# Performance work log

Hardware: AMD Instinct MI355X
Metric: run time of the kernel (lower is better)

The kernel has to match this reference:

```python
import jax, jax.numpy as jnp
from jax import lax
import numpy as np

B, L, D = 2048, 100, 64      # batch, max_len, embedding_dim
K = 64                       # embedding_num (codebook entries)
CB = K * 8                   # code_book_dim = 512 (== D*8 encoder out channels)
ITEMS = 1_000_000
EPS = 1e-3                   # tf.layers.batch_normalization default epsilon


def setup_inputs() -> dict:
    key = jax.random.key(0)
    ks = jax.random.split(key, 16)
    w = lambda i, shape: jax.random.normal(ks[i], shape, dtype=jnp.float32) * 0.05
    z = lambda c: jnp.zeros((c,), jnp.float32)
    o = lambda c: jnp.ones((c,), jnp.float32)
    return {
        "history_item_ids": jax.random.randint(ks[0], (B, L), 0, ITEMS, dtype=jnp.int32),
        "history_item_masks": jax.random.randint(ks[1], (B, L), 0, 2, dtype=jnp.int32),
        "item_embedding_table": jax.random.normal(ks[2], (ITEMS, D), dtype=jnp.float32),
        "user_book": jax.random.normal(ks[3], (K, CB), dtype=jnp.float32),
        "e_w1": w(4, (2, 2, D, 2 * D)), "e_b1": z(2 * D), "e_g1": o(2 * D), "e_be1": z(2 * D),
        "e_w2": w(5, (2, 2, 2 * D, 4 * D)), "e_b2": z(4 * D), "e_g2": o(4 * D), "e_be2": z(4 * D),
        "e_w3": w(6, (2, 2, 4 * D, 8 * D)), "e_b3": z(8 * D),
        "d_w1": w(7, (2, 2, 8 * D, 4 * D)), "d_b1": z(4 * D), "d_g1": o(4 * D), "d_be1": z(4 * D),
        "d_w2": w(8, (2, 2, 4 * D, 2 * D)), "d_b2": z(2 * D), "d_g2": o(2 * D), "d_be2": z(2 * D),
        "d_w3": w(9, (2, 2, 2 * D, D)), "d_b3": z(D),
    }


def _forward(history_item_ids, history_item_masks, item_embedding_table, user_book,
             e_w1, e_b1, e_g1, e_be1, e_w2, e_b2, e_g2, e_be2, e_w3, e_b3,
             d_w1, d_b1, d_g1, d_be1, d_w2, d_b2, d_g2, d_be2, d_w3, d_b3):
    dn = ('NHWC', 'HWIO', 'NHWC')
    bn = lambda x, g, b: x * (g / jnp.sqrt(1.0 + EPS)) + b  # inference BN: moving mean 0, var 1
    conv = lambda x, w_, b_: lax.conv_general_dilated(x, w_, (1, 1), 'VALID', dimension_numbers=dn) + b_
    deconv = lambda x, w_, b_: lax.conv_transpose(x, w_, (1, 1), 'VALID', dimension_numbers=dn) + b_

    mask = (history_item_masks >= 1).astype(jnp.float32)               # [B,L]
    hist = item_embedding_table[history_item_ids] * mask[..., None]    # [B,L,D]

    H = int(L ** 0.5); W = L // H
    h = hist.reshape(-1, H, W, D)
    h = jax.nn.relu(bn(conv(h, e_w1, e_b1), e_g1, e_be1))              # [B,9,9,2D]
    h = jax.nn.relu(bn(conv(h, e_w2, e_b2), e_g2, e_be2))              # [B,8,8,4D]
    x_encode = conv(h, e_w3, e_b3)                                     # [B,7,7,CB]

    # nearest-neighbor codebook lookup (get_quantized)
    flat = x_encode.reshape(-1, CB)                                    # [B*49,CB]
    dist = ((flat * flat).sum(1, keepdims=True)
            + (user_book * user_book).sum(1)
            - 2.0 * flat @ user_book.T)                                # [B*49,K]
    idx = jnp.argmin(dist, axis=1)
    quantized = user_book[idx].reshape(x_encode.shape)                 # [B,7,7,CB]

    # straight-through estimator
    st = x_encode + lax.stop_gradient(quantized - x_encode)
    g = jax.nn.relu(bn(deconv(st, d_w1, d_b1), d_g1, d_be1))           # [B,8,8,4D]
    g = jax.nn.relu(bn(deconv(g, d_w2, d_b2), d_g2, d_be2))            # [B,9,9,2D]
    vq_x = deconv(g, d_w3, d_b3).reshape(hist.shape)                   # [B,L,D]

    vq_mean = vq_x.sum(1) / mask.sum(-1, keepdims=True)                # [B,D]
    mse = lambda a, b: jnp.mean((a - b) ** 2)
    beta = 0.25
    vqvae_loss = (mse(hist, vq_x)
                  + mse(quantized, lax.stop_gradient(x_encode))
                  + beta * mse(x_encode, lax.stop_gradient(quantized)))
    return vq_mean, vq_x, vqvae_loss


def reference(history_item_ids, history_item_masks, item_embedding_table, user_book,
              e_w1, e_b1, e_g1, e_be1, e_w2, e_b2, e_g2, e_be2, e_w3, e_b3,
              d_w1, d_b1, d_g1, d_be1, d_w2, d_b2, d_g2, d_be2, d_w3, d_b3):
    return _forward(history_item_ids, history_item_masks, item_embedding_table, user_book,
                    e_w1, e_b1, e_g1, e_be1, e_w2, e_b2, e_g2, e_be2, e_w3, e_b3,
                    d_w1, d_b1, d_g1, d_be1, d_w2, d_b2, d_g2, d_be2, d_w3, d_b3)
```

## Files before the change

### kernel.cpp

```cpp
#include <hip/hip_runtime.h>
#include <hip/hip_bf16.h>
#include <cstdint>
#include <cstddef>


typedef __attribute__((ext_vector_type(8))) short short8v;
typedef __attribute__((ext_vector_type(4))) float f32x4;

constexpr int B  = 2048;
constexpr int L  = 100;
constexpr int K  = 64;
constexpr int CB = 512;
#define MARGIN 0.1f

constexpr size_t R0_OFF  = 0;
constexpr size_t R1_OFF  = 51380224;
constexpr size_t IDX_OFF = 84934656;
constexpr size_t CBN_OFF = 85035008;
constexpr size_t CNT_OFF = 85035072;
constexpr size_t ACC_OFF = 85035088;
constexpr size_t WL_OFF  = 85035104;
constexpr size_t WB_OFF  = 85135456;

constexpr size_t EW1H=0,       EW1L=32768;
constexpr size_t EW2H=65536,   EW2L=196608;
constexpr size_t EW3H=327680;
constexpr size_t DW2H=851968,  DW3H=983040;
constexpr size_t W3BH=1015808, W3BL=1081344;
constexpr size_t WB_USH_END=1146880;

constexpr size_t BW1_OFF  = WB_OFF + 573440;
constexpr size_t DOTB_OFF = BW1_OFF + 65536;

__device__ inline ushort bf16_hi(float f){ __hip_bfloat16 h=__float2bfloat16(f); return *(ushort*)&h; }
__device__ inline float  bf16_tof(ushort u){ __hip_bfloat16 h; *(ushort*)&h=u; return __bfloat162float(h); }

__device__ void wtrans(const float* __restrict__ w, int IC, int OC,
                       ushort* __restrict__ hi, ushort* __restrict__ lo,
                       int gid, int gsz)
{
    int tot = 4*IC*OC;
    for (int i = gid; i < tot; i += gsz) {
        int kk = i/(IC*OC), r = i - kk*(IC*OC), ic = r/OC, oc = r - ic*OC;
        float v = w[i];
        ushort h = bf16_hi(v);
        size_t dst = ((size_t)kk*OC + oc)*IC + ic;
        hi[dst] = h;
        if (lo) lo[dst] = bf16_hi(v - bf16_tof(h));
    }
}

__global__ __launch_bounds__(256)
void wprep_k(const float* e1, const float* e2, const float* e3,
             const float* d2, const float* d3, ushort* wb)
{
    int gid = blockIdx.x*256 + threadIdx.x, gsz = gridDim.x*256;
    wtrans(e1,  64, 128, wb+EW1H, wb+EW1L, gid, gsz);
    wtrans(e2, 128, 256, wb+EW2H, wb+EW2L, gid, gsz);
    wtrans(e3, 256, 512, wb+EW3H, nullptr, gid, gsz);
    wtrans(d2, 256, 128, wb+DW2H, nullptr, gid, gsz);
    wtrans(d3, 128,  64, wb+DW3H, nullptr, gid, gsz);
}

__global__ __launch_bounds__(256)
void w3b_k(const float* __restrict__ e_w3, const float* __restrict__ book,
           ushort* __restrict__ wb)
{
    const int kk = blockIdx.x >> 6, k = blockIdx.x & 63, ic = threadIdx.x;
    const float4* wr = (const float4*)(e_w3 + ((size_t)(kk*256)+ic)*512);
    const float4* br = (const float4*)(book + (size_t)k*512);
    float s = 0.f;
    for (int c = 0; c < 128; ++c) {
        float4 a = wr[c], bb = br[c];
        s = fmaf(a.x,bb.x,fmaf(a.y,bb.y,fmaf(a.z,bb.z,fmaf(a.w,bb.w,s))));
    }
    size_t dst = ((size_t)(kk*64+k))*256 + ic;
    ushort h = bf16_hi(s);
    wb[W3BH+dst] = h;
    wb[W3BL+dst] = bf16_hi(s - bf16_tof(h));
}

__global__ __launch_bounds__(256)
void bw1_k(const float* __restrict__ d_w1, const float* __restrict__ book,
           float* __restrict__ bw1)
{
    const int tap = blockIdx.x >> 6, k = blockIdx.x & 63, oc = threadIdx.x;
    const float* br = book + (size_t)k*512;
    const float* wr = d_w1 + (size_t)(tap*512)*256 + oc;
    float s = 0.f;
    for (int ic = 0; ic < 512; ++ic)
        s = fmaf(br[ic], wr[(size_t)ic*256], s);
    bw1[((size_t)(tap*64+k))*256 + oc] = s;
}

__global__ __launch_bounds__(256)
void prep_k(const float* __restrict__ book, const float* __restrict__ e_b3,
            float* __restrict__ cbn, float* __restrict__ dotb,
            float* __restrict__ acc, int* __restrict__ cnt)
{
    const int t = threadIdx.x;
    if (t < 64) {
        const float* r = book + t * 512;
        float s = 0.f, d = 0.f;
        for (int c = 0; c < 512; ++c) { s = fmaf(r[c], r[c], s); d = fmaf(e_b3[c], r[c], d); }
        cbn[t] = s; dotb[t] = d;
    }
    if (t == 64 || t == 65) acc[t-64] = 0.f;
    if (t == 66) *cnt = 0;
}

template<int IH,int IW,int IC,int OC,int PAD,int MODE,bool HASBN,bool SPLIT,
         int OCS,int ICC,int MT,int OUTFMT,bool FUSE>
__global__ __launch_bounds__(256)
void sconv_k(const uint* __restrict__ in_pk, const ushort* __restrict__ in_bf,
             const int* __restrict__ ids, const int* __restrict__ masks,
             const float* __restrict__ table,
             const ushort* __restrict__ wt_hi, const ushort* __restrict__ wt_lo,
             const float* __restrict__ bias, const float* __restrict__ gamma,
             const float* __restrict__ beta,
             float* __restrict__ out_f, uint* __restrict__ out_pk,
             ushort* __restrict__ out_bf, float* __restrict__ out_mean,
             float* __restrict__ acc_g)
{
    constexpr int OH=IH+2*PAD-1, OW=IW+2*PAD-1, NPOS=OH*OW, IHW=IH*IW;
    constexpr int OCB=OC/OCS, NPW=OCB/4, NT=NPW/16;
    constexpr int NCH=IC/ICC, KS=ICC/32;
    constexpr int PL=SPLIT?2:1;
    constexpr int NB=(NCH>1)?2:1;
    constexpr int AROWS=IHW+1, RB=ICC*2;
    constexpr int C8=ICC/8;
    constexpr int NITEMS=IHW*C8;
    constexpr int SI=(NITEMS+255)/256;
    constexpr bool EXACT=(SI*256==NITEMS);
    constexpr int BUFB=PL*AROWS*RB;

    __shared__ ushort s_a[NB*PL*AROWS*ICC];
    char* sb=(char*)s_a;

    const int v=blockIdx.x, r8=v&7, iv=v>>3;
    const int b = r8*(B/8) + iv/OCS;
    const int sl = iv - (iv/OCS)*OCS;

    const int tid=threadIdx.x, lane=tid&63, wv=tid>>6;
    const int l15=lane&15, lq=lane>>4;
    const int n0=sl*OCB + wv*NPW;

    int arow[4][MT];
    #pragma unroll
    for(int kk=0;kk<4;++kk){
        const int ky=kk>>1, kx=kk&1;
        #pragma unroll
        for(int m=0;m<MT;++m){
            int p=m*16+l15;
            int py=p/OW, px=p-py*OW;
            int ty=py+ky-PAD, tx=px+kx-PAD;
            bool ok=(p<NPOS)&&((unsigned)ty<(unsigned)IH)&&((unsigned)tx<(unsigned)IW);
            arow[kk][m]= ok ? ty*IW+tx : IHW;
        }
    }

    f32x4 acc[MT][NT];
    #pragma unroll
    for(int m=0;m<MT;++m)
        #pragma unroll
        for(int n=0;n<NT;++n) acc[m][n]=(f32x4)0.0f;

    uint4 r0[SI];
    uint4 r1[(MODE==1||MODE==3)?SI:1];
    float msk[(MODE==1)?SI:1];

    auto stage_load=[&](int c){
        const int ic0=c*ICC;
        #pragma unroll
        for(int t=0;t<SI;++t){
            int idx=tid+t*256;
            if(EXACT || idx<NITEMS){
                int row=idx/C8, g=idx-row*C8;
                if constexpr(MODE==1){
                    int id=ids[b*L+row];
                    msk[t]=(masks[b*L+row]>=1)?1.f:0.f;
                    const float* src=table+(size_t)id*64+g*8;
                    r0[t]=*(const uint4*)src;
                    r1[t]=*(const uint4*)(src+4);
                } else if constexpr(MODE==3){
                    const uint* src=in_pk+((size_t)b*IHW+row)*IC+ic0+g*8;
                    r0[t]=*(const uint4*)src;
                    r1[t]=*(const uint4*)(src+4);
                } else {
                    r0[t]=*(const uint4*)(in_bf+((size_t)b*IHW+row)*IC+ic0+g*8);
                }
            }
        }
    };

    auto stage_write=[&](int bufb){
        #pragma unroll
        for(int t=0;t<SI;++t){
            int idx=tid+t*256;
            if(EXACT || idx<NITEMS){
                int row=idx/C8, g=idx-row*C8;
                int boff=bufb + row*RB + ((g^(row&7))<<4);
                if constexpr(MODE==1){
                    const float* f0=(const float*)&r0[t];
                    const float* f1=(const float*)&r1[t];
                    float vv[8]={f0[0]*msk[t],f0[1]*msk[t],f0[2]*msk[t],f0[3]*msk[t],
                                 f1[0]*msk[t],f1[1]*msk[t],f1[2]*msk[t],f1[3]*msk[t]};
                    ushort hh[8], ll[8];
                    #pragma unroll
                    for(int j=0;j<8;++j){ hh[j]=bf16_hi(vv[j]); ll[j]=bf16_hi(vv[j]-bf16_tof(hh[j])); }
                    *(uint4*)(sb+boff)=*(uint4*)hh;
                    *(uint4*)(sb+AROWS*RB+boff)=*(uint4*)ll;
                } else if constexpr(MODE==3){
                    const uint* u0=(const uint*)&r0[t];
                    const uint* u1=(const uint*)&r1[t];
                    ushort hh[8], ll[8];
                    #pragma unroll
                    for(int j=0;j<4;++j){ hh[j]=(ushort)(u0[j]&0xffffu); ll[j]=(ushort)(u0[j]>>16); }
                    #pragma unroll
                    for(int j=0;j<4;++j){ hh[4+j]=(ushort)(u1[j]&0xffffu); ll[4+j]=(ushort)(u1[j]>>16); }
                    *(uint4*)(sb+boff)=*(uint4*)hh;
                    *(uint4*)(sb+AROWS*RB+boff)=*(uint4*)ll;
                } else {
                    *(uint4*)(sb+boff)=r0[t];
                }
            }
        }
    };

    stage_load(0);
    stage_write(0);
    for(int z=tid; z<NB*PL*C8; z+=256){
        int nb=z/(PL*C8), rz=z-nb*(PL*C8), pl=rz/C8, g=rz-pl*C8;
        *(uint4*)(sb + nb*BUFB + pl*(AROWS*RB) + IHW*RB + (g<<4)) = make_uint4(0,0,0,0);
    }
    __syncthreads();

    for(int c=0;c<NCH;++c){
        if(c+1<NCH) stage_load(c+1);
        const int bufb=(c&1)*BUFB;
        const int ic0=c*ICC;
        __builtin_amdgcn_s_setprio(1);
        #pragma unroll
        for(int kk=0;kk<4;++kk){
            #pragma unroll
            for(int ks=0;ks<KS;++ks){
                short8v bhv[NT]; short8v blv[SPLIT?NT:1];
                #pragma unroll
                for(int n=0;n<NT;++n){
                    int col=n0+n*16+l15;
                    size_t widx=((size_t)kk*OC+col)*IC+ic0+ks*32+lq*8;
                    bhv[n]=*(const short8v*)(wt_hi+widx);
                    if constexpr(SPLIT) blv[n]=*(const short8v*)(wt_lo+widx);
                }
                #pragma unroll
                for(int m=0;m<MT;++m){
                    int off=bufb + arow[kk][m]*RB + ((((ks<<2)|lq)^(arow[kk][m]&7))<<4);
                    short8v ah=*(const short8v*)(sb+off);
                    if constexpr(SPLIT){
                        short8v al=*(const short8v*)(sb+AROWS*RB+off);
                        #pragma unroll
                        for(int n=0;n<NT;++n){
                            acc[m][n]=__builtin_amdgcn_mfma_f32_16x16x32_bf16(ah,bhv[n],acc[m][n],0,0,0);
                            acc[m][n]=__builtin_amdgcn_mfma_f32_16x16x32_bf16(ah,blv[n],acc[m][n],0,0,0);
                            acc[m][n]=__builtin_amdgcn_mfma_f32_16x16x32_bf16(al,bhv[n],acc[m][n],0,0,0);
                        }
                    } else {
                        #pragma unroll
                        for(int n=0;n<NT;++n)
                            acc[m][n]=__builtin_amdgcn_mfma_f32_16x16x32_bf16(ah,bhv[n],acc[m][n],0,0,0);
                    }
                }
            }
        }
        __builtin_amdgcn_s_setprio(0);
        if(c+1<NCH){
            stage_write(((c+1)&1)*BUFB);
            __syncthreads();
        }
    }

    const float rs=(float)(1.0/sqrt(1.0+1e-3));
    float lsum=0.f, colsum=0.f;
    #pragma unroll
    for(int n=0;n<NT;++n){
        int col=n0+n*16+l15;
        float bi=bias[col];
        float gsc=0.f, bt=0.f;
        if constexpr(HASBN){ gsc=gamma[col]*rs; bt=beta[col]; }
        #pragma unroll
        for(int m=0;m<MT;++m){
            #pragma unroll
            for(int j=0;j<4;++j){
                int p=m*16+lq*4+j;
                if(p<NPOS){
                    float vx=acc[m][n][j]+bi;
                    if constexpr(HASBN) vx=fmaxf(fmaf(vx,gsc,bt),0.f);
                    size_t g=(size_t)b*NPOS+p;
                    if constexpr(OUTFMT==0){
                        out_f[g*OC+col]=vx;
                    } else if constexpr(OUTFMT==1){
                        ushort h=bf16_hi(vx);
                        ushort lo=bf16_hi(vx-bf16_tof(h));
                        out_pk[g*OC+col]=(uint)h | ((uint)lo<<16);
                    } else {
                        out_bf[g*OC+col]=bf16_hi(vx);
                    }
                    if constexpr(FUSE){
                        int id=ids[b*L+p];
                        float mm=(masks[b*L+p]>=1)?1.f:0.f;
                        float h=table[(size_t)id*64+col]*mm;
                        float df=h-vx;
                        lsum=fmaf(df,df,lsum);
                        colsum+=vx;
                    }
                }
            }
        }
    }

    if constexpr(FUSE){
        float mc=0.f;
        for(int l=lane;l<L;l+=64) mc += (masks[b*L+l]>=1)?1.f:0.f;
        #pragma unroll
        for(int off=32;off;off>>=1) mc+=__shfl_xor(mc,off);
        colsum += __shfl_xor(colsum,16);
        colsum += __shfl_xor(colsum,32);
        if(lq==0) out_mean[b*64 + n0 + l15] = colsum/mc;
        #pragma unroll
        for(int off=32;off;off>>=1) lsum+=__shfl_xor(lsum,off);
        __syncthreads();
        float* red=(float*)sb;
        if(lane==0) red[wv]=lsum;
        __syncthreads();
        if(tid==0) atomicAdd(acc_g+0, red[0]+red[1]+red[2]+red[3]);
    }
}

template<bool DOT>
__global__ __launch_bounds__(256)
void xnd_k(const uint* __restrict__ in_pk,
           const ushort* __restrict__ wx,
           const ushort* __restrict__ w3bh, const ushort* __restrict__ w3bl,
           const float* __restrict__ xbias,
           const float* __restrict__ cbn, const float* __restrict__ dotb,
           int* __restrict__ qidx, float* __restrict__ acc_g,
           int* __restrict__ cnt, int* __restrict__ wl)
{
    constexpr int IHW=64, AROWS=65, RB=128, NCH=4, C8=8;
    constexpr int NPOS=49, OW=7, MT=4, NT=4;
    constexpr int PLX=DOT?2:1;
    constexpr int BUFB=PLX*AROWS*RB;

    __shared__ ushort s_a[2*PLX*AROWS*64];
    char* sb=(char*)s_a;

    const int v=blockIdx.x;
    const int b=(v&7)*(B/8)+(v>>3);
    const int tid=threadIdx.x, lane=tid&63, wv=tid>>6;
    const int l15=lane&15, lq=lane>>4;
    const int n0x=(DOT?0:256)+wv*64;

    int arow[4][MT];
    #pragma unroll
    for(int kk=0;kk<4;++kk){
        const int ky=kk>>1, kx=kk&1;
        #pragma unroll
        for(int m=0;m<MT;++m){
            int p=m*16+l15;
            int py=p/OW, px=p-py*OW;
            bool ok=(p<NPOS);
            arow[kk][m]= ok ? (py+ky)*8+(px+kx) : IHW;
        }
    }

    f32x4 accx[MT][NT];
    #pragma unroll
    for(int m=0;m<MT;++m)
        #pragma unroll
        for(int n=0;n<NT;++n) accx[m][n]=(f32x4)0.0f;
    f32x4 accd[DOT?MT:1];
    #pragma unroll
    for(int m=0;m<(DOT?MT:1);++m) accd[m]=(f32x4)0.0f;

    uint4 r0[2], r1[2];

    auto stage_load=[&](int c){
        const int ic0=c*64;
        #pragma unroll
        for(int t=0;t<2;++t){
            int idx=tid+t*256;
            int row=idx>>3, g=idx&7;
            const uint* src=in_pk+((size_t)b*IHW+row)*256+ic0+g*8;
            r0[t]=*(const uint4*)src;
            r1[t]=*(const uint4*)(src+4);
        }
    };
    auto stage_write=[&](int bufb){
        #pragma unroll
        for(int t=0;t<2;++t){
            int idx=tid+t*256;
            int row=idx>>3, g=idx&7;
            int boff=bufb + row*RB + ((g^(row&7))<<4);
            const uint* u0=(const uint*)&r0[t];
            const uint* u1=(const uint*)&r1[t];
            ushort hh[8];
            #pragma unroll
            for(int j=0;j<4;++j){ hh[j]=(ushort)(u0[j]&0xffffu); hh[4+j]=(ushort)(u1[j]&0xffffu); }
            *(uint4*)(sb+boff)=*(uint4*)hh;
            if constexpr(DOT){
                ushort ll[8];
                #pragma unroll
                for(int j=0;j<4;++j){ ll[j]=(ushort)(u0[j]>>16); ll[4+j]=(ushort)(u1[j]>>16); }
                *(uint4*)(sb+AROWS*RB+boff)=*(uint4*)ll;
            }
        }
    };

    stage_load(0);
    stage_write(0);
    for(int z=tid; z<2*PLX*C8; z+=256){
        int nb=z/(PLX*C8), rz=z-nb*(PLX*C8), pl=rz/C8, g=rz-pl*C8;
        *(uint4*)(sb + nb*BUFB + pl*(AROWS*RB) + IHW*RB + (g<<4)) = make_uint4(0,0,0,0);
    }
    __syncthreads();

    for(int c=0;c<NCH;++c){
        if(c+1<NCH) stage_load(c+1);
        const int bufb=(c&1)*BUFB;
        const int ic0=c*64;
        __builtin_amdgcn_s_setprio(1);
        #pragma unroll
        for(int kk=0;kk<4;++kk){
            #pragma unroll
            for(int ks=0;ks<2;++ks){
                short8v bx[NT];
                #pragma unroll
                for(int n=0;n<NT;++n){
                    int col=n0x+n*16+l15;
                    bx[n]=*(const short8v*)(wx+((size_t)kk*512+col)*256+ic0+ks*32+lq*8);
                }
                short8v bdh, bdl;
                if constexpr(DOT){
                    int cold=wv*16+l15;
                    size_t wdx=((size_t)kk*64+cold)*256+ic0+ks*32+lq*8;
                    bdh=*(const short8v*)(w3bh+wdx);
                    bdl=*(const short8v*)(w3bl+wdx);
                }
                #pragma unroll
                for(int m=0;m<MT;++m){
                    int off=bufb + arow[kk][m]*RB + ((((ks<<2)|lq)^(arow[kk][m]&7))<<4);
                    short8v ah=*(const short8v*)(sb+off);
                    #pragma unroll
                    for(int n=0;n<NT;++n)
                        accx[m][n]=__builtin_amdgcn_mfma_f32_16x16x32_bf16(ah,bx[n],accx[m][n],0,0,0);
                    if constexpr(DOT){
                        short8v al=*(const short8v*)(sb+AROWS*RB+off);
                        accd[m]=__builtin_amdgcn_mfma_f32_16x16x32_bf16(ah,bdh,accd[m],0,0,0);
                        accd[m]=__builtin_amdgcn_mfma_f32_16x16x32_bf16(ah,bdl,accd[m],0,0,0);
                        accd[m]=__builtin_amdgcn_mfma_f32_16x16x32_bf16(al,bdh,accd[m],0,0,0);
                    }
                }
            }
        }
        __builtin_amdgcn_s_setprio(0);
        if(c+1<NCH){
            stage_write(((c+1)&1)*BUFB);
            __syncthreads();
        }
    }

    float xs=0.f;
    #pragma unroll
    for(int n=0;n<NT;++n){
        int col=n0x+n*16+l15;
        float bi=xbias[col];
        #pragma unroll
        for(int m=0;m<MT;++m){
            #pragma unroll
            for(int j=0;j<4;++j){
                int p=m*16+lq*4+j;
                if(p<NPOS){ float vv=accx[m][n][j]+bi; xs=fmaf(vv,vv,xs); }
            }
        }
    }
    #pragma unroll
    for(int off=32;off;off>>=1) xs+=__shfl_xor(xs,off);
    __syncthreads();
    float* f=(float*)sb;
    if(lane==0) f[wv]=xs;

    if constexpr(DOT){
        float cb=cbn[wv*16+l15], db=dotb[wv*16+l15];
        float* sd1=f+8;
        int*   sk =(int*)(f+8+256);
        float* sd2=f+8+512;
        #pragma unroll
        for(int m=0;m<MT;++m){
            #pragma unroll
            for(int j=0;j<4;++j){
                int p=m*16+lq*4+j;
                float d1=cb-2.f*(accd[m][j]+db);
                int   k1=wv*16+l15;
                float d2=3.4e38f;
                #pragma unroll
                for(int off=1;off<16;off<<=1){
                    float od1=__shfl_xor(d1,off);
                    int   ok1=__shfl_xor(k1,off);
                    float od2=__shfl_xor(d2,off);
                    if(od1<d1 || (od1==d1 && ok1<k1)){ d2=fminf(d1,od2); d1=od1; k1=ok1; }
                    else                              { d2=fminf(d2,od1); }
                }
                if(l15==0){ sd1[p*4+wv]=d1; sk[p*4+wv]=k1; sd2[p*4+wv]=d2; }
            }
        }
    }
    __syncthreads();
    if(tid==0) atomicAdd(acc_g+1, f[0]+f[1]+f[2]+f[3]);

    if constexpr(DOT){
        float* sd1=f+8;
        int*   sk =(int*)(f+8+256);
        float* sd2=f+8+512;
        float lsum=0.f;
        if(tid<NPOS){
            float d1=sd1[tid*4+0]; int k1=sk[tid*4+0]; float d2=sd2[tid*4+0];
            #pragma unroll
            for(int w=1;w<4;++w){
                float D1=sd1[tid*4+w]; int K1=sk[tid*4+w]; float D2=sd2[tid*4+w];
                if(D1<d1){ d2=fminf(d1,D2); d1=D1; k1=K1; }
                else     { d2=fminf(d2,D1); }
            }
            qidx[b*49+tid]=k1;
            if(d2-d1<=MARGIN){ int t=atomicAdd(cnt,1); wl[t]=b*49+tid; }
            lsum=d1;
        }
        if(tid<64){
            #pragma unroll
            for(int off=32;off;off>>=1) lsum+=__shfl_xor(lsum,off);
            if(lane==0) atomicAdd(acc_g+1, lsum);
        }
    }
}

__global__ __launch_bounds__(256)
void dgather_k(const int* __restrict__ qidx, const float* __restrict__ bw1,
               const float* __restrict__ b1, const float* __restrict__ g1s,
               const float* __restrict__ be1, ushort* __restrict__ G1)
{
    const int b=blockIdx.x, tid=threadIdx.x;
    const int pg=tid>>2, og=(tid&3)*64;
    const int py=pg>>3, px=pg&7;

    float a[64];
    #pragma unroll
    for(int j=0;j<64;++j) a[j]=0.f;

    #pragma unroll
    for(int tap=0;tap<4;++tap){
        int iy=py+(tap>>1)-1, ix=px+(tap&1)-1;
        if((unsigned)iy<7u && (unsigned)ix<7u){
            int kq=qidx[b*49+iy*7+ix];
            const float4* src=(const float4*)(bw1+((size_t)(tap*64+kq))*256+og);
            #pragma unroll
            for(int j=0;j<16;++j){
                float4 vv=src[j];
                a[4*j+0]+=vv.x; a[4*j+1]+=vv.y; a[4*j+2]+=vv.z; a[4*j+3]+=vv.w;
            }
        }
    }
    const float rs=(float)(1.0/sqrt(1.0+1e-3));
    #pragma unroll
    for(int j=0;j<64;++j){
        int col=og+j;
        float vv=a[j]+b1[col];
        vv=fmaxf(fmaf(vv, g1s[col]*rs, be1[col]), 0.f);
        G1[((size_t)b*64+pg)*256+col]=bf16_hi(vv);
    }
}

__global__ __launch_bounds__(256)
void recompute_k(const int* __restrict__ wl, const int* __restrict__ cnt,
                 const int* __restrict__ ids, const int* __restrict__ masks,
                 const float* __restrict__ table, const float* __restrict__ book,
                 const float* __restrict__ e_w1, const float* __restrict__ e_b1,
                 const float* __restrict__ e_g1, const float* __restrict__ e_be1,
                 const float* __restrict__ e_w2, const float* __restrict__ e_b2,
                 const float* __restrict__ e_g2, const float* __restrict__ e_be2,
                 const float* __restrict__ e_w3, const float* __restrict__ e_b3,
                 int* __restrict__ qidx)
{
    __shared__ double s_h[16*64];
    __shared__ double s_a1[9*128];
    __shared__ double s_a2[4*256];
    __shared__ double s_x[512];
    __shared__ double s_d[256];

    const int tid = threadIdx.x;
    const double rs = 1.0 / sqrt(1.0 + 1e-3);
    const int n = *cnt;

    for (int wi = blockIdx.x; wi < n; wi += gridDim.x) {
        const int row = wl[wi];
        const int b = row / 49, p = row % 49;
        const int py = p / 7, px = p % 7;

        for (int i = tid; i < 16*64; i += 256) {
            int cell = i >> 6, d = i & 63;
            int l = (py + (cell >> 2)) * 10 + (px + (cell & 3));
            int id = ids[b*100 + l];
            double m = (masks[b*100 + l] >= 1) ? 1.0 : 0.0;
            s_h[i] = (double)table[(size_t)id*64 + d] * m;
        }
        __syncthreads();

        for (int i = tid; i < 9*128; i += 256) {
            int cell = i >> 7, oc = i & 127;
            int ry = cell / 3, rx = cell % 3;
            double s = 0.0;
            #pragma unroll
            for (int kk = 0; kk < 4; ++kk) {
                int icell = (ry + (kk>>1))*4 + (rx + (kk&1));
                const double* hh = s_h + icell*64;
                const float* ww = e_w1 + (kk*64)*128 + oc;
                for (int ic = 0; ic < 64; ++ic)
                    s = fma(hh[ic], (double)ww[ic*128], s);
            }
            s += (double)e_b1[oc];
            s = s * ((double)e_g1[oc] * rs) + (double)e_be1[oc];
            s_a1[i] = s > 0.0 ? s : 0.0;
        }
        __syncthreads();

        for (int i = tid; i < 4*256; i += 256) {
            int cell = i >> 8, oc = i & 255;
            int qy = cell >> 1, qx = cell & 1;
            double s = 0.0;
            #pragma unroll
            for (int kk = 0; kk < 4; ++kk) {
                int icell = (qy + (kk>>1))*3 + (qx + (kk&1));
                const double* aa = s_a1 + icell*128;
                const float* ww = e_w2 + (kk*128)*256 + oc;
                for (int ic = 0; ic < 128; ++ic)
                    s = fma(aa[ic], (double)ww[ic*256], s);
            }
            s += (double)e_b2[oc];
            s = s * ((double)e_g2[oc] * rs) + (double)e_be2[oc];
            s_a2[i] = s > 0.0 ? s : 0.0;
        }
        __syncthreads();

        for (int i = tid; i < 512; i += 256) {
            double s = 0.0;
            #pragma unroll
            for (int kk = 0; kk < 4; ++kk) {
                const double* aa = s_a2 + kk*256;
                const float* ww = e_w3 + (kk*256)*512 + i;
                for (int ic = 0; ic < 256; ++ic)
                    s = fma(aa[ic], (double)ww[ic*512], s);
            }
            s_x[i] = s + (double)e_b3[i];
        }
        __syncthreads();

        {
            int k = tid & 63, seg = tid >> 6;
            const float* cr = book + k*512 + seg*128;
            const double* xr = s_x + seg*128;
            double s = 0.0;
            for (int c = 0; c < 128; ++c) {
                double dd = xr[c] - (double)cr[c];
                s = fma(dd, dd, s);
            }
            s_d[seg*64 + k] = s;
        }
        __syncthreads();

        if (tid < 64) {
            double dv = s_d[tid] + s_d[64+tid] + s_d[128+tid] + s_d[192+tid];
            int kk2 = tid;
            #pragma unroll
            for (int off = 32; off > 0; off >>= 1) {
                double od = __shfl_xor(dv, off);
                int    ok = __shfl_xor(kk2, off);
                if (od < dv || (od == dv && ok < kk2)) { dv = od; kk2 = ok; }
            }
            if (tid == 0) qidx[row] = kk2;
        }
        __syncthreads();
    }
}

__global__ void loss_k(const float* __restrict__ acc, float* __restrict__ out_loss)
{
    float l1 = acc[0] / 13107200.f;
    float l2 = acc[1] / 51380224.f;
    out_loss[0] = l1 + l2 + 0.25f * l2;
}

extern "C" void kernel_launch(void* const* d_in, const int* in_sizes, int n_in,
                              void* d_out, int out_size, void* d_ws, size_t ws_size,
                              hipStream_t stream)
{
    const int*   ids   = (const int*)d_in[0];
    const int*   masks = (const int*)d_in[1];
    const float* table = (const float*)d_in[2];
    const float* book  = (const float*)d_in[3];
    const float* e_w1  = (const float*)d_in[4];
    const float* e_b1  = (const float*)d_in[5];
    const float* e_g1  = (const float*)d_in[6];
    const float* e_be1 = (const float*)d_in[7];
    const float* e_w2  = (const float*)d_in[8];
    const float* e_b2  = (const float*)d_in[9];
    const float* e_g2  = (const float*)d_in[10];
    const float* e_be2 = (const float*)d_in[11];
    const float* e_w3  = (const float*)d_in[12];
    const float* e_b3  = (const float*)d_in[13];
    const float* d_w1  = (const float*)d_in[14];
    const float* d_b1  = (const float*)d_in[15];
    const float* d_g1  = (const float*)d_in[16];
    const float* d_be1 = (const float*)d_in[17];
    const float* d_w2  = (const float*)d_in[18];
    const float* d_b2  = (const float*)d_in[19];
    const float* d_g2  = (const float*)d_in[20];
    const float* d_be2 = (const float*)d_in[21];
    const float* d_w3  = (const float*)d_in[22];
    const float* d_b3  = (const float*)d_in[23];

    float*  ws  = (float*)d_ws;
    uint*   A1P = (uint*)(ws + R0_OFF);
    uint*   A2P = (uint*)(ws + R1_OFF);
    ushort* G1  = (ushort*)(ws + R1_OFF);
    ushort* G2  = (ushort*)(ws + R0_OFF);
    int*    IDX = (int*)(ws + IDX_OFF);
    float*  CBN = ws + CBN_OFF;
    int*    CNT = (int*)(ws + CNT_OFF);
    float*  ACC = ws + ACC_OFF;
    int*    WL  = (int*)(ws + WL_OFF);
    ushort* WB  = (ushort*)(ws + WB_OFF);
    float*  BW1 = ws + BW1_OFF;
    float*  DOTB= ws + DOTB_OFF;

    float* out_mean = (float*)d_out;
    float* out_vqx  = (float*)d_out + (size_t)B * 64;
    float* out_loss = (float*)d_out + (size_t)B * 64 + (size_t)B * L * 64;

    prep_k<<<1, 256, 0, stream>>>(book, e_b3, CBN, DOTB, ACC, CNT);
    wprep_k<<<512, 256, 0, stream>>>(e_w1, e_w2, e_w3, d_w2, d_w3, WB);
    w3b_k<<<256, 256, 0, stream>>>(e_w3, book, WB);
    bw1_k<<<256, 256, 0, stream>>>(d_w1, book, BW1);

    sconv_k<10,10, 64,128,0,1,true ,true ,1, 64,6,1,false><<<B,   256,0,stream>>>(
        nullptr, nullptr, ids, masks, table,
        WB+EW1H, WB+EW1L, e_b1, e_g1, e_be1, nullptr, A1P, nullptr, nullptr, nullptr);
    sconv_k< 9, 9,128,256,0,3,true ,true ,2, 64,4,1,false><<<B*2, 256,0,stream>>>(
        A1P, nullptr, nullptr, nullptr, nullptr,
        WB+EW2H, WB+EW2L, e_b2, e_g2, e_be2, nullptr, A2P, nullptr, nullptr, nullptr);

    xnd_k<true ><<<B, 256, 0, stream>>>(A2P, WB+EW3H, WB+W3BH, WB+W3BL,
                                        e_b3, CBN, DOTB, IDX, ACC, CNT, WL);
    xnd_k<false><<<B, 256, 0, stream>>>(A2P, WB+EW3H, nullptr, nullptr,
                                        e_b3, nullptr, nullptr, nullptr, ACC, nullptr, nullptr);

    recompute_k<<<512, 256, 0, stream>>>(WL, CNT, ids, masks, table, book,
                                         e_w1, e_b1, e_g1, e_be1,
                                         e_w2, e_b2, e_g2, e_be2,
                                         e_w3, e_b3, IDX);

    dgather_k<<<B, 256, 0, stream>>>(IDX, BW1, d_b1, d_g1, d_be1, G1);
    sconv_k< 8, 8,256,128,1,4,true ,false,1, 64,6,2,false><<<B,   256,0,stream>>>(
        nullptr, G1, nullptr, nullptr, nullptr,
        WB+DW2H, nullptr, d_b2, d_g2, d_be2, nullptr, nullptr, G2, nullptr, nullptr);
    sconv_k< 9, 9,128, 64,1,4,false,false,1, 64,7,0,true ><<<B,   256,0,stream>>>(
        nullptr, G2, ids, masks, table,
        WB+DW3H, nullptr, d_b3, nullptr, nullptr, out_vqx, nullptr, nullptr, out_mean, ACC);

    loss_k<<<1, 1, 0, stream>>>(ACC, out_loss);
}
```

Baseline: 1.221 ms.

## Process multiple samples per conv block and merge encoder-final kernels

Adds an SMP template parameter so each sconv block handles several batch samples, reusing each loaded weight fragment across them. It also adds a DBUF option to fall back to single-buffered LDS. It is applied to encoder conv2 (now single-buffered) and decoder conv2. The two xnd_k launches are merged into one 512-thread kernel in which waves 0-3 also compute the codebook dot products. This cuts weight reloads and reads the shared activation once, at the cost of more accumulator registers, more LDS per block and fewer blocks.

Result: slower. 1.310 ms (+7.3%).

```diff
diff --git a/kernel.cpp b/kernel.cpp
--- a/kernel.cpp
+++ b/kernel.cpp
@@ -27,7 +27,6 @@
 constexpr size_t EW3H=327680;
 constexpr size_t DW2H=851968,  DW3H=983040;
 constexpr size_t W3BH=1015808, W3BL=1081344;
-constexpr size_t WB_USH_END=1146880;
 
 constexpr size_t BW1_OFF  = WB_OFF + 573440;
 constexpr size_t DOTB_OFF = BW1_OFF + 65536;
@@ -110,7 +109,7 @@
 }
 
 template<int IH,int IW,int IC,int OC,int PAD,int MODE,bool HASBN,bool SPLIT,
-         int OCS,int ICC,int MT,int OUTFMT,bool FUSE>
+         int OCS,int ICC,int MT,int OUTFMT,bool FUSE,int SMP,bool DBUF>
 __global__ __launch_bounds__(256)
 void sconv_k(const uint* __restrict__ in_pk, const ushort* __restrict__ in_bf,
              const int* __restrict__ ids, const int* __restrict__ masks,
@@ -126,19 +125,21 @@
     constexpr int OCB=OC/OCS, NPW=OCB/4, NT=NPW/16;
     constexpr int NCH=IC/ICC, KS=ICC/32;
     constexpr int PL=SPLIT?2:1;
-    constexpr int NB=(NCH>1)?2:1;
+    constexpr int NB=(DBUF && NCH>1)?2:1;
     constexpr int AROWS=IHW+1, RB=ICC*2;
     constexpr int C8=ICC/8;
-    constexpr int NITEMS=IHW*C8;
+    constexpr int NITEMS=SMP*IHW*C8;
     constexpr int SI=(NITEMS+255)/256;
     constexpr bool EXACT=(SI*256==NITEMS);
-    constexpr int BUFB=PL*AROWS*RB;
-
-    __shared__ ushort s_a[NB*PL*AROWS*ICC];
+    constexpr int SPLB=AROWS*RB;
+    constexpr int SAMB=PL*SPLB;
+    constexpr int BUFB=SMP*SAMB;
+
+    __shared__ ushort s_a[NB*SMP*PL*AROWS*ICC];
     char* sb=(char*)s_a;
 
     const int v=blockIdx.x, r8=v&7, iv=v>>3;
-    const int b = r8*(B/8) + iv/OCS;
+    const int b0 = (r8*(B/SMP/8) + iv/OCS)*SMP;
     const int sl = iv - (iv/OCS)*OCS;
 
     const int tid=threadIdx.x, lane=tid&63, wv=tid>>6;
@@ -159,11 +160,13 @@
         }
     }
 
-    f32x4 acc[MT][NT];
-    #pragma unroll
-    for(int m=0;m<MT;++m)
-        #pragma unroll
-        for(int n=0;n<NT;++n) acc[m][n]=(f32x4)0.0f;
+    f32x4 acc[SMP][MT][NT];
+    #pragma unroll
+    for(int s=0;s<SMP;++s)
+        #pragma unroll
+        for(int m=0;m<MT;++m)
+            #pragma unroll
+            for(int n=0;n<NT;++n) acc[s][m][n]=(f32x4)0.0f;
 
     uint4 r0[SI];
     uint4 r1[(MODE==1||MODE==3)?SI:1];
@@ -176,18 +179,19 @@
             int idx=tid+t*256;
             if(EXACT || idx<NITEMS){
                 int row=idx/C8, g=idx-row*C8;
+                int s=row/IHW, r=row-s*IHW;
                 if constexpr(MODE==1){
-                    int id=ids[b*L+row];
-                    msk[t]=(masks[b*L+row]>=1)?1.f:0.f;
+                    int id=ids[(b0+s)*L+r];
+                    msk[t]=(masks[(b0+s)*L+r]>=1)?1.f:0.f;
                     const float* src=table+(size_t)id*64+g*8;
                     r0[t]=*(const uint4*)src;
                     r1[t]=*(const uint4*)(src+4);
                 } else if constexpr(MODE==3){
-                    const uint* src=in_pk+((size_t)b*IHW+row)*IC+ic0+g*8;
+                    const uint* src=in_pk+((size_t)(b0+s)*IHW+r)*IC+ic0+g*8;
                     r0[t]=*(const uint4*)src;
                     r1[t]=*(const uint4*)(src+4);
                 } else {
-                    r0[t]=*(const uint4*)(in_bf+((size_t)b*IHW+row)*IC+ic0+g*8);
+                    r0[t]=*(const uint4*)(in_bf+((size_t)(b0+s)*IHW+r)*IC+ic0+g*8);
                 }
             }
         }
@@ -199,7 +203,8 @@
             int idx=tid+t*256;
             if(EXACT || idx<NITEMS){
                 int row=idx/C8, g=idx-row*C8;
-                int boff=bufb + row*RB + ((g^(row&7))<<4);
+                int s=row/IHW, r=row-s*IHW;
+                int boff=bufb + s*SAMB + r*RB + ((g^(r&7))<<4);
                 if constexpr(MODE==1){
                     const float* f0=(const float*)&r0[t];
                     const float* f1=(const float*)&r1[t];
@@ -209,7 +214,7 @@
                     #pragma unroll
                     for(int j=0;j<8;++j){ hh[j]=bf16_hi(vv[j]); ll[j]=bf16_hi(vv[j]-bf16_tof(hh[j])); }
                     *(uint4*)(sb+boff)=*(uint4*)hh;
-                    *(uint4*)(sb+AROWS*RB+boff)=*(uint4*)ll;
+                    *(uint4*)(sb+SPLB+boff)=*(uint4*)ll;
                 } else if constexpr(MODE==3){
                     const uint* u0=(const uint*)&r0[t];
                     const uint* u1=(const uint*)&r1[t];
@@ -219,7 +224,7 @@
                     #pragma unroll
                     for(int j=0;j<4;++j){ hh[4+j]=(ushort)(u1[j]&0xffffu); ll[4+j]=(ushort)(u1[j]>>16); }
                     *(uint4*)(sb+boff)=*(uint4*)hh;
-                    *(uint4*)(sb+AROWS*RB+boff)=*(uint4*)ll;
+                    *(uint4*)(sb+SPLB+boff)=*(uint4*)ll;
                 } else {
                     *(uint4*)(sb+boff)=r0[t];
                 }
@@ -227,17 +232,15 @@
         }
     };
 
-    stage_load(0);
-    stage_write(0);
-    for(int z=tid; z<NB*PL*C8; z+=256){
-        int nb=z/(PL*C8), rz=z-nb*(PL*C8), pl=rz/C8, g=rz-pl*C8;
-        *(uint4*)(sb + nb*BUFB + pl*(AROWS*RB) + IHW*RB + (g<<4)) = make_uint4(0,0,0,0);
-    }
-    __syncthreads();
-
-    for(int c=0;c<NCH;++c){
-        if(c+1<NCH) stage_load(c+1);
-        const int bufb=(c&1)*BUFB;
+    auto zero_rows=[&](){
+        for(int z=tid; z<NB*SMP*PL*C8; z+=256){
+            int nb=z/(SMP*PL*C8), rz=z-nb*(SMP*PL*C8);
+            int s=rz/(PL*C8), rz2=rz-s*(PL*C8), pl=rz2/C8, g=rz2-pl*C8;
+            *(uint4*)(sb + nb*BUFB + s*SAMB + pl*SPLB + IHW*RB + (g<<4)) = make_uint4(0,0,0,0);
+        }
+    };
+
+    auto do_mfma=[&](int bufb, int c){
         const int ic0=c*ICC;
         __builtin_amdgcn_s_setprio(1);
         #pragma unroll
@@ -253,72 +256,102 @@
                     if constexpr(SPLIT) blv[n]=*(const short8v*)(wt_lo+widx);
                 }
                 #pragma unroll
-                for(int m=0;m<MT;++m){
-                    int off=bufb + arow[kk][m]*RB + ((((ks<<2)|lq)^(arow[kk][m]&7))<<4);
-                    short8v ah=*(const short8v*)(sb+off);
-                    if constexpr(SPLIT){
-                        short8v al=*(const short8v*)(sb+AROWS*RB+off);
-                        #pragma unroll
-                        for(int n=0;n<NT;++n){
-                            acc[m][n]=__builtin_amdgcn_mfma_f32_16x16x32_bf16(ah,bhv[n],acc[m][n],0,0,0);
-                            acc[m][n]=__builtin_amdgcn_mfma_f32_16x16x32_bf16(ah,blv[n],acc[m][n],0,0,0);
-                            acc[m][n]=__builtin_amdgcn_mfma_f32_16x16x32_bf16(al,bhv[n],acc[m][n],0,0,0);
+                for(int s=0;s<SMP;++s){
+                    const int sbase=bufb + s*SAMB;
+                    #pragma unroll
+                    for(int m=0;m<MT;++m){
+                        int off=sbase + arow[kk][m]*RB + ((((ks<<2)|lq)^(arow[kk][m]&7))<<4);
+                        short8v ah=*(const short8v*)(sb+off);
+                        if constexpr(SPLIT){
+                            short8v al=*(const short8v*)(sb+SPLB+off);
+                            #pragma unroll
+                            for(int n=0;n<NT;++n){
+                                acc[s][m][n]=__builtin_amdgcn_mfma_f32_16x16x32_bf16(ah,bhv[n],acc[s][m][n],0,0,0);
+                                acc[s][m][n]=__builtin_amdgcn_mfma_f32_16x16x32_bf16(ah,blv[n],acc[s][m][n],0,0,0);
+                                acc[s][m][n]=__builtin_amdgcn_mfma_f32_16x16x32_bf16(al,bhv[n],acc[s][m][n],0,0,0);
+                            }
+                        } else {
+                            #pragma unroll
+                            for(int n=0;n<NT;++n)
+                                acc[s][m][n]=__builtin_amdgcn_mfma_f32_16x16x32_bf16(ah,bhv[n],acc[s][m][n],0,0,0);
                         }
-                    } else {
-                        #pragma unroll
-                        for(int n=0;n<NT;++n)
-                            acc[m][n]=__builtin_amdgcn_mfma_f32_16x16x32_bf16(ah,bhv[n],acc[m][n],0,0,0);
                     }
                 }
             }
         }
         __builtin_amdgcn_s_setprio(0);
-        if(c+1<NCH){
-            stage_write(((c+1)&1)*BUFB);
+    };
+
+    if constexpr(NB==1){
+        stage_load(0);
+        zero_rows();
+        for(int c=0;c<NCH;++c){
+            if(c) __syncthreads();
+            stage_write(0);
             __syncthreads();
+            if(c+1<NCH) stage_load(c+1);
+            do_mfma(0,c);
+        }
+    } else {
+        stage_load(0);
+        stage_write(0);
+        zero_rows();
+        __syncthreads();
+        for(int c=0;c<NCH;++c){
+            if(c+1<NCH) stage_load(c+1);
+            do_mfma((c&1)*BUFB,c);
+            if(c+1<NCH){
+                stage_write(((c+1)&1)*BUFB);
+                __syncthreads();
+            }
         }
     }
 
     const float rs=(float)(1.0/sqrt(1.0+1e-3));
     float lsum=0.f, colsum=0.f;
     #pragma unroll
-    for(int n=0;n<NT;++n){
-        int col=n0+n*16+l15;
-        float bi=bias[col];
-        float gsc=0.f, bt=0.f;
-        if constexpr(HASBN){ gsc=gamma[col]*rs; bt=beta[col]; }
-        #pragma unroll
-        for(int m=0;m<MT;++m){
-            #pragma unroll
-            for(int j=0;j<4;++j){
-                int p=m*16+lq*4+j;
-                if(p<NPOS){
-                    float vx=acc[m][n][j]+bi;
-                    if constexpr(HASBN) vx=fmaxf(fmaf(vx,gsc,bt),0.f);
-                    size_t g=(size_t)b*NPOS+p;
-                    if constexpr(OUTFMT==0){
-                        out_f[g*OC+col]=vx;
-                    } else if constexpr(OUTFMT==1){
-                        ushort h=bf16_hi(vx);
-                        ushort lo=bf16_hi(vx-bf16_tof(h));
-                        out_pk[g*OC+col]=(uint)h | ((uint)lo<<16);
-                    } else {
-                        out_bf[g*OC+col]=bf16_hi(vx);
+    for(int s=0;s<SMP;++s){
+        const int b=b0+s;
+        #pragma unroll
+        for(int n=0;n<NT;++n){
+            int col=n0+n*16+l15;
+            float bi=bias[col];
+            float gsc=0.f, bt=0.f;
+            if constexpr(HASBN){ gsc=gamma[col]*rs; bt=beta[col]; }
+            #pragma unroll
+            for(int m=0;m<MT;++m){
+                #pragma unroll
+                for(int j=0;j<4;++j){
+                    int p=m*16+lq*4+j;
+                    if(p<NPOS){
+                        float vx=acc[s][m][n][j]+bi;
+                        if constexpr(HASBN) vx=fmaxf(fmaf(vx,gsc,bt),0.f);
+                        size_t g=(size_t)b*NPOS+p;
+                        if constexpr(OUTFMT==0){
+                            out_f[g*OC+col]=vx;
+                        } else if constexpr(OUTFMT==1){
+                            ushort h=bf16_hi(vx);
+                            ushort lo=bf16_hi(vx-bf16_tof(h));
+                            out_pk[g*OC+col]=(uint)h | ((uint)lo<<16);
+                        } else {
+                            out_bf[g*OC+col]=bf16_hi(vx);
+                        }
+                        if constexpr(FUSE){
+                            int id=ids[b*L+p];
+                            float mm=(masks[b*L+p]>=1)?1.f:0.f;
+                            float h=table[(size_t)id*64+col]*mm;
+                            float df=h-vx;
+                            lsum=fmaf(df,df,lsum);
+                            colsum+=vx;
+                        }
                     }
-                    if constexpr(FUSE){
-                        int id=ids[b*L+p];
-                        float mm=(masks[b*L+p]>=1)?1.f:0.f;
-                        float h=table[(size_t)id*64+col]*mm;
-                        float df=h-vx;
-                        lsum=fmaf(df,df,lsum);
-                        colsum+=vx;
-                    }
                 }
             }
         }
     }
 
     if constexpr(FUSE){
+        const int b=b0;
         float mc=0.f;
         for(int l=lane;l<L;l+=64) mc += (masks[b*L+l]>=1)?1.f:0.f;
         #pragma unroll
@@ -336,29 +369,28 @@
     }
 }
 
-template<bool DOT>
-__global__ __launch_bounds__(256)
-void xnd_k(const uint* __restrict__ in_pk,
-           const ushort* __restrict__ wx,
-           const ushort* __restrict__ w3bh, const ushort* __restrict__ w3bl,
-           const float* __restrict__ xbias,
-           const float* __restrict__ cbn, const float* __restrict__ dotb,
-           int* __restrict__ qidx, float* __restrict__ acc_g,
-           int* __restrict__ cnt, int* __restrict__ wl)
-{
-    constexpr int IHW=64, AROWS=65, RB=128, NCH=4, C8=8;
+__global__ __launch_bounds__(512)
+void mxnd_k(const uint* __restrict__ in_pk,
+            const ushort* __restrict__ wx,
+            const ushort* __restrict__ w3bh, const ushort* __restrict__ w3bl,
+            const float* __restrict__ xbias,
+            const float* __restrict__ cbn, const float* __restrict__ dotb,
+            int* __restrict__ qidx, float* __restrict__ acc_g,
+            int* __restrict__ cnt, int* __restrict__ wl)
+{
+    constexpr int IHW=64, AROWS=65, RB=128;
     constexpr int NPOS=49, OW=7, MT=4, NT=4;
-    constexpr int PLX=DOT?2:1;
-    constexpr int BUFB=PLX*AROWS*RB;
-
-    __shared__ ushort s_a[2*PLX*AROWS*64];
+    constexpr int SPLB=AROWS*RB;
+    constexpr int BUFB=2*SPLB;
+
+    __shared__ ushort s_a[2*2*AROWS*64];
     char* sb=(char*)s_a;
 
     const int v=blockIdx.x;
     const int b=(v&7)*(B/8)+(v>>3);
     const int tid=threadIdx.x, lane=tid&63, wv=tid>>6;
     const int l15=lane&15, lq=lane>>4;
-    const int n0x=(DOT?0:256)+wv*64;
+    const int n0x=wv*64;
 
     int arow[4][MT];
     #pragma unroll
@@ -368,8 +400,7 @@
         for(int m=0;m<MT;++m){
             int p=m*16+l15;
             int py=p/OW, px=p-py*OW;
-            bool ok=(p<NPOS);
-            arow[kk][m]= ok ? (py+ky)*8+(px+kx) : IHW;
+            arow[kk][m]= (p<NPOS) ? (py+ky)*8+(px+kx) : IHW;
         }
     }
 
@@ -378,54 +409,43 @@
     for(int m=0;m<MT;++m)
         #pragma unroll
         for(int n=0;n<NT;++n) accx[m][n]=(f32x4)0.0f;
-    f32x4 accd[DOT?MT:1];
-    #pragma unroll
-    for(int m=0;m<(DOT?MT:1);++m) accd[m]=(f32x4)0.0f;
-
-    uint4 r0[2], r1[2];
+    f32x4 accd[MT];
+    #pragma unroll
+    for(int m=0;m<MT;++m) accd[m]=(f32x4)0.0f;
+
+    uint4 r0, r1;
 
     auto stage_load=[&](int c){
         const int ic0=c*64;
-        #pragma unroll
-        for(int t=0;t<2;++t){
-            int idx=tid+t*256;
-            int row=idx>>3, g=idx&7;
-            const uint* src=in_pk+((size_t)b*IHW+row)*256+ic0+g*8;
-            r0[t]=*(const uint4*)src;
-            r1[t]=*(const uint4*)(src+4);
-        }
+        int row=tid>>3, g=tid&7;
+        const uint* src=in_pk+((size_t)b*IHW+row)*256+ic0+g*8;
+        r0=*(const uint4*)src;
+        r1=*(const uint4*)(src+4);
     };
     auto stage_write=[&](int bufb){
-        #pragma unroll
-        for(int t=0;t<2;++t){
-            int idx=tid+t*256;
-            int row=idx>>3, g=idx&7;
-            int boff=bufb + row*RB + ((g^(row&7))<<4);
-            const uint* u0=(const uint*)&r0[t];
-            const uint* u1=(const uint*)&r1[t];
-            ushort hh[8];
-            #pragma unroll
-            for(int j=0;j<4;++j){ hh[j]=(ushort)(u0[j]&0xffffu); hh[4+j]=(ushort)(u1[j]&0xffffu); }
-            *(uint4*)(sb+boff)=*(uint4*)hh;
-            if constexpr(DOT){
-                ushort ll[8];
-                #pragma unroll
-                for(int j=0;j<4;++j){ ll[j]=(ushort)(u0[j]>>16); ll[4+j]=(ushort)(u1[j]>>16); }
-                *(uint4*)(sb+AROWS*RB+boff)=*(uint4*)ll;
-            }
-        }
+        int row=tid>>3, g=tid&7;
+        int boff=bufb + row*RB + ((g^(row&7))<<4);
+        const uint* u0=(const uint*)&r0;
+        const uint* u1=(const uint*)&r1;
+        ushort hh[8], ll[8];
+        #pragma unroll
+        for(int j=0;j<4;++j){ hh[j]=(ushort)(u0[j]&0xffffu); ll[j]=(ushort)(u0[j]>>16); }
+        #pragma unroll
+        for(int j=0;j<4;++j){ hh[4+j]=(ushort)(u1[j]&0xffffu); ll[4+j]=(ushort)(u1[j]>>16); }
+        *(uint4*)(sb+boff)=*(uint4*)hh;
+        *(uint4*)(sb+SPLB+boff)=*(uint4*)ll;
     };
 
     stage_load(0);
     stage_write(0);
-    for(int z=tid; z<2*PLX*C8; z+=256){
-        int nb=z/(PLX*C8), rz=z-nb*(PLX*C8), pl=rz/C8, g=rz-pl*C8;
-        *(uint4*)(sb + nb*BUFB + pl*(AROWS*RB) + IHW*RB + (g<<4)) = make_uint4(0,0,0,0);
+    for(int z=tid; z<2*2*8; z+=512){
+        int nb=z/16, rz=z-nb*16, pl=rz/8, g=rz-pl*8;
+        *(uint4*)(sb + nb*BUFB + pl*SPLB + IHW*RB + (g<<4)) = make_uint4(0,0,0,0);
     }
     __syncthreads();
 
-    for(int c=0;c<NCH;++c){
-        if(c+1<NCH) stage_load(c+1);
+    for(int c=0;c<4;++c){
+        if(c+1<4) stage_load(c+1);
         const int bufb=(c&1)*BUFB;
         const int ic0=c*64;
         __builtin_amdgcn_s_setprio(1);
@@ -440,7 +460,7 @@
                     bx[n]=*(const short8v*)(wx+((size_t)kk*512+col)*256+ic0+ks*32+lq*8);
                 }
                 short8v bdh, bdl;
-                if constexpr(DOT){
+                if(wv<4){
                     int cold=wv*16+l15;
                     size_t wdx=((size_t)kk*64+cold)*256+ic0+ks*32+lq*8;
                     bdh=*(const short8v*)(w3bh+wdx);
@@ -453,8 +473,8 @@
                     #pragma unroll
                     for(int n=0;n<NT;++n)
                         accx[m][n]=__builtin_amdgcn_mfma_f32_16x16x32_bf16(ah,bx[n],accx[m][n],0,0,0);
-                    if constexpr(DOT){
-                        short8v al=*(const short8v*)(sb+AROWS*RB+off);
+                    if(wv<4){
+                        short8v al=*(const short8v*)(sb+SPLB+off);
                         accd[m]=__builtin_amdgcn_mfma_f32_16x16x32_bf16(ah,bdh,accd[m],0,0,0);
                         accd[m]=__builtin_amdgcn_mfma_f32_16x16x32_bf16(ah,bdl,accd[m],0,0,0);
                         accd[m]=__builtin_amdgcn_mfma_f32_16x16x32_bf16(al,bdh,accd[m],0,0,0);
@@ -463,7 +483,7 @@
             }
         }
         __builtin_amdgcn_s_setprio(0);
-        if(c+1<NCH){
+        if(c+1<4){
             stage_write(((c+1)&1)*BUFB);
             __syncthreads();
         }
@@ -489,11 +509,11 @@
     float* f=(float*)sb;
     if(lane==0) f[wv]=xs;
 
-    if constexpr(DOT){
+    if(wv<4){
         float cb=cbn[wv*16+l15], db=dotb[wv*16+l15];
-        float* sd1=f+8;
-        int*   sk =(int*)(f+8+256);
-        float* sd2=f+8+512;
+        float* sd1=f+16;
+        int*   sk =(int*)(f+16+256);
+        float* sd2=f+16+512;
         #pragma unroll
         for(int m=0;m<MT;++m){
             #pragma unroll
@@ -510,17 +530,17 @@
                     if(od1<d1 || (od1==d1 && ok1<k1)){ d2=fminf(d1,od2); d1=od1; k1=ok1; }
                     else                              { d2=fminf(d2,od1); }
                 }
-                if(l15==0){ sd1[p*4+wv]=d1; sk[p*4+wv]=k1; sd2[p*4+wv]=d2; }
+                if(l15==0 && p<NPOS){ sd1[p*4+wv]=d1; sk[p*4+wv]=k1; sd2[p*4+wv]=d2; }
             }
         }
     }
     __syncthreads();
-    if(tid==0) atomicAdd(acc_g+1, f[0]+f[1]+f[2]+f[3]);
-
-    if constexpr(DOT){
-        float* sd1=f+8;
-        int*   sk =(int*)(f+8+256);
-        float* sd2=f+8+512;
+    if(tid==0) atomicAdd(acc_g+1, f[0]+f[1]+f[2]+f[3]+f[4]+f[5]+f[6]+f[7]);
+
+    {
+        float* sd1=f+16;
+        int*   sk =(int*)(f+16+256);
+        float* sd2=f+16+512;
         float lsum=0.f;
         if(tid<NPOS){
             float d1=sd1[tid*4+0]; int k1=sk[tid*4+0]; float d2=sd2[tid*4+0];
@@ -537,7 +557,7 @@
         if(tid<64){
             #pragma unroll
             for(int off=32;off;off>>=1) lsum+=__shfl_xor(lsum,off);
-            if(lane==0) atomicAdd(acc_g+1, lsum);
+            if(tid==0) atomicAdd(acc_g+1, lsum);
         }
     }
 }
@@ -749,17 +769,15 @@
     w3b_k<<<256, 256, 0, stream>>>(e_w3, book, WB);
     bw1_k<<<256, 256, 0, stream>>>(d_w1, book, BW1);
 
-    sconv_k<10,10, 64,128,0,1,true ,true ,1, 64,6,1,false><<<B,   256,0,stream>>>(
+    sconv_k<10,10, 64,128,0,1,true ,true ,1, 64,6,1,false,1,true ><<<B,    256,0,stream>>>(
         nullptr, nullptr, ids, masks, table,
         WB+EW1H, WB+EW1L, e_b1, e_g1, e_be1, nullptr, A1P, nullptr, nullptr, nullptr);
-    sconv_k< 9, 9,128,256,0,3,true ,true ,2, 64,4,1,false><<<B*2, 256,0,stream>>>(
+    sconv_k< 9, 9,128,256,0,3,true ,true ,2, 64,4,1,false,2,false><<<B,    256,0,stream>>>(
         A1P, nullptr, nullptr, nullptr, nullptr,
         WB+EW2H, WB+EW2L, e_b2, e_g2, e_be2, nullptr, A2P, nullptr, nullptr, nullptr);
 
-    xnd_k<true ><<<B, 256, 0, stream>>>(A2P, WB+EW3H, WB+W3BH, WB+W3BL,
-                                        e_b3, CBN, DOTB, IDX, ACC, CNT, WL);
-    xnd_k<false><<<B, 256, 0, stream>>>(A2P, WB+EW3H, nullptr, nullptr,
-                                        e_b3, nullptr, nullptr, nullptr, ACC, nullptr, nullptr);
+    mxnd_k<<<B, 512, 0, stream>>>(A2P, WB+EW3H, WB+W3BH, WB+W3BL,
+                                  e_b3, CBN, DOTB, IDX, ACC, CNT, WL);
 
     recompute_k<<<512, 256, 0, stream>>>(WL, CNT, ids, masks, table, book,
                                          e_w1, e_b1, e_g1, e_be1,
@@ -767,10 +785,10 @@
                                          e_w3, e_b3, IDX);
 
     dgather_k<<<B, 256, 0, stream>>>(IDX, BW1, d_b1, d_g1, d_be1, G1);
-    sconv_k< 8, 8,256,128,1,4,true ,false,1, 64,6,2,false><<<B,   256,0,stream>>>(
+    sconv_k< 8, 8,256,128,1,4,true ,false,1, 64,6,2,false,2,true ><<<B/2,  256,0,stream>>>(
         nullptr, G1, nullptr, nullptr, nullptr,
         WB+DW2H, nullptr, d_b2, d_g2, d_be2, nullptr, nullptr, G2, nullptr, nullptr);
-    sconv_k< 9, 9,128, 64,1,4,false,false,1, 64,7,0,true ><<<B,   256,0,stream>>>(
+    sconv_k< 9, 9,128, 64,1,4,false,false,1, 64,7,0,true ,1,true ><<<B,    256,0,stream>>>(
         nullptr, G2, ids, masks, table,
         WB+DW3H, nullptr, d_b3, nullptr, nullptr, out_vqx, nullptr, nullptr, out_mean, ACC);
 
```
